# Performance work log

Hardware: AMD Instinct MI355X
Metric: run time of the kernel (lower is better)

## Reference

```python
import jax, jax.numpy as jnp
import numpy as np

B, NQ, NN, EMB, H, D = 64, 256, 512, 128, 8, 16
SQRT_EMB = float(np.sqrt(EMB))
LOGIT_CLIP = 10.0


def setup_inputs() -> dict:
    key = jax.random.key(0)
    ks = jax.random.split(key, 9)
    encoded_last_node = jax.random.normal(ks[0], (B, NQ, EMB), jnp.float32)
    attr = jax.random.uniform(ks[1], (B, NQ, 1), jnp.float32)  # e.g. remaining load in [0,1]
    encoded_nodes = jax.random.normal(ks[2], (B, NN, EMB), jnp.float32)
    ninf_mask = jnp.where(jax.random.uniform(ks[3], (B, NQ, NN)) < 0.15,
                          -jnp.inf, 0.0).astype(jnp.float32)
    def lin(k, fan_in, fan_out):
        lim = 1.0 / np.sqrt(fan_in)
        return jax.random.uniform(k, (fan_in, fan_out), jnp.float32, -lim, lim)
    Wq_last = lin(ks[4], EMB + 1, H * D)
    Wk = lin(ks[5], EMB, H * D)
    Wv = lin(ks[6], EMB, H * D)
    Wcomb = lin(ks[7], H * D, EMB)
    bcomb = jax.random.uniform(ks[8], (EMB,), jnp.float32, -1.0 / np.sqrt(H * D), 1.0 / np.sqrt(H * D))
    return dict(encoded_last_node=encoded_last_node, attr=attr,
                encoded_nodes=encoded_nodes, ninf_mask=ninf_mask,
                Wq_last=Wq_last, Wk=Wk, Wv=Wv, Wcomb=Wcomb, bcomb=bcomb)


def _heads(x):  # [B, T, H*D] -> [B, H, T, D]
    return x.reshape(x.shape[0], x.shape[1], H, D).transpose(0, 2, 1, 3)


def reference(encoded_last_node, attr, encoded_nodes, ninf_mask,
              Wq_last, Wk, Wv, Wcomb, bcomb):
    # fix fully-masked rows: un-mask index 0 (matches torch mask_inf patch)
    all_inf = jnp.isinf(ninf_mask).all(axis=2)  # [B, NQ]
    ninf_mask = ninf_mask.at[:, :, 0].set(jnp.where(all_inf, 0.0, ninf_mask[:, :, 0]))

    # set_kv
    k = _heads(encoded_nodes @ Wk)  # [B,H,NN,D]
    v = _heads(encoded_nodes @ Wv)  # [B,H,NN,D]

    # q from last node + attr
    q = _heads(jnp.concatenate([encoded_last_node, attr], axis=2) @ Wq_last)  # [B,H,NQ,D]

    # masked multi-head attention
    score = jnp.einsum('bhnd,bhmd->bhnm', q, k) / jnp.sqrt(jnp.float32(D))
    score = score + ninf_mask[:, None, :, :]          # rank3 mask broadcast over heads
    weights = jax.nn.softmax(score, axis=-1)          # [B,H,NQ,NN]
    out = jnp.einsum('bhnm,bhmd->bhnd', weights, v)
    out_concat = out.transpose(0, 2, 1, 3).reshape(B, NQ, H * D)
    mh_atten_out = out_concat @ Wcomb + bcomb         # [B,NQ,EMB]

    # single-head compatibility score + tanh clip + mask + softmax
    score2 = jnp.einsum('bne,bme->bnm', mh_atten_out, encoded_nodes) / SQRT_EMB
    logits = LOGIT_CLIP * jnp.tanh(score2) + ninf_mask
    probs = jax.nn.softmax(logits, axis=2)            # [B,NQ,NN]
    return probs
```

## Files before the change

kernel.cpp:

```cpp
#include <hip/hip_runtime.h>
#include <math.h>

#define NB    64
#define NQn   256
#define NNn   512
#define HDn   128
#define LOG2E 1.44269504088896340736f
#define INV_SQRT_EMB 0.08838834764831845f

__device__ __forceinline__ float4 ldg4(const float* p) {
    return *reinterpret_cast<const float4*>(p);
}

__global__ __launch_bounds__(256, 2)
void proj_kernel(const float* __restrict__ X,
                 const float* __restrict__ W0, const float* __restrict__ W1,
                 const float* __restrict__ wrow, const float* __restrict__ attr,
                 const float* __restrict__ bias,
                 float* __restrict__ Y0, float* __restrict__ Y1)
{
    __shared__ float Xs[64 * 128];
    __shared__ float Wt[64 * 128];
    const int tid = threadIdx.x;
    const int rg = tid >> 4;
    const int cg = tid & 15;
    const int rowblk = blockIdx.x * 64;
    const int colbase = blockIdx.y * 64;

    #pragma unroll
    for (int i = 0; i < 8; ++i) {
        int idx = tid + 256 * i;
        int r = idx >> 5;
        int c4 = idx & 31;
        float4 v = ldg4(X + (rowblk + r) * 128 + c4 * 4);
        *reinterpret_cast<float4*>(&Xs[r * 128 + ((c4 ^ (r & 7)) << 2)]) = v;
    }

    for (int pass = 0; pass < 2; ++pass) {
        if (pass && (W1 == nullptr)) break;
        const float* W = pass ? W1 : W0;
        float* Y = pass ? Y1 : Y0;
        __syncthreads();
        #pragma unroll
        for (int i = 0; i < 32; ++i) {
            int idx = tid + 256 * i;
            int k = idx >> 6;
            int c = idx & 63;
            float w = W[k * 128 + colbase + c];
            Wt[c * 128 + ((((k >> 2) ^ (c & 7)) << 2) | (k & 3))] = w;
        }
        __syncthreads();

        float acc[4][4];
        #pragma unroll
        for (int r = 0; r < 4; ++r)
            #pragma unroll
            for (int c = 0; c < 4; ++c) acc[r][c] = 0.f;

        const int rsw = rg & 7;
        const int csw = cg & 7;
        #pragma unroll 8
        for (int k4 = 0; k4 < 32; ++k4) {
            float4 a[4], bv[4];
            #pragma unroll
            for (int r = 0; r < 4; ++r)
                a[r] = *reinterpret_cast<const float4*>(&Xs[(rg + 16 * r) * 128 + ((k4 ^ rsw) << 2)]);
            #pragma unroll
            for (int c = 0; c < 4; ++c)
                bv[c] = *reinterpret_cast<const float4*>(&Wt[(cg + 16 * c) * 128 + ((k4 ^ csw) << 2)]);
            #pragma unroll
            for (int r = 0; r < 4; ++r)
                #pragma unroll
                for (int c = 0; c < 4; ++c)
                    acc[r][c] += a[r].x * bv[c].x + a[r].y * bv[c].y
                               + a[r].z * bv[c].z + a[r].w * bv[c].w;
        }

        if (attr != nullptr) {
            #pragma unroll
            for (int r = 0; r < 4; ++r) {
                float av = attr[rowblk + rg + 16 * r];
                #pragma unroll
                for (int c = 0; c < 4; ++c)
                    acc[r][c] += av * wrow[colbase + cg + 16 * c];
            }
        }
        #pragma unroll
        for (int r = 0; r < 4; ++r) {
            int row = rowblk + rg + 16 * r;
            #pragma unroll
            for (int c = 0; c < 4; ++c) {
                int col = colbase + cg + 16 * c;
                float o = acc[r][c];
                if (bias != nullptr) o += bias[col];
                Y[row * 128 + col] = o;
            }
        }
    }
}

__global__ __launch_bounds__(512, 4)
void attn_kernel(const float* __restrict__ Q, const float* __restrict__ K,
                 const float* __restrict__ V, const float* __restrict__ mask,
                 float* __restrict__ P0, float* __restrict__ P1,
                 float* __restrict__ L0, float* __restrict__ L1)
{
    __shared__ float Ks[32 * 128];
    __shared__ float Vs[32 * 128];
    __shared__ float Ms[32 * 64];
    const int tid  = threadIdx.x;
    const int lane = tid & 63;
    const int h    = tid >> 6;
    const int b    = blockIdx.x;
    const int qt   = blockIdx.y;
    const int ns   = blockIdx.z;
    const int q    = qt * 64 + lane;
    const int nb   = ns * 256;

    float qv[16];
    {
        const float* qp = Q + (b * NQn + q) * 128 + h * 16;
        const float sc = 0.25f * LOG2E;
        float4 t0 = ldg4(qp), t1 = ldg4(qp + 4), t2 = ldg4(qp + 8), t3 = ldg4(qp + 12);
        qv[0]=t0.x*sc;  qv[1]=t0.y*sc;  qv[2]=t0.z*sc;  qv[3]=t0.w*sc;
        qv[4]=t1.x*sc;  qv[5]=t1.y*sc;  qv[6]=t1.z*sc;  qv[7]=t1.w*sc;
        qv[8]=t2.x*sc;  qv[9]=t2.y*sc;  qv[10]=t2.z*sc; qv[11]=t2.w*sc;
        qv[12]=t3.x*sc; qv[13]=t3.y*sc; qv[14]=t3.z*sc; qv[15]=t3.w*sc;
    }

    float out[16];
    #pragma unroll
    for (int d = 0; d < 16; ++d) out[d] = 0.f;
    float lsum = 0.f;

    const int srow = tid >> 3;
    const int sn4  = tid & 7;

    for (int t = 0; t < 8; ++t) {
        const int n0 = nb + t * 32;
        __syncthreads();
        {
            int i0 = tid, i1 = tid + 512;
            const float* kg = K + (b * NNn + n0) * 128;
            const float* vg = V + (b * NNn + n0) * 128;
            float4 k0 = ldg4(kg + i0 * 4), k1 = ldg4(kg + i1 * 4);
            float4 v0 = ldg4(vg + i0 * 4), v1 = ldg4(vg + i1 * 4);
            float4 mk = ldg4(mask + (b * NQn + qt * 64 + srow) * NNn + n0 + sn4 * 4);
            *reinterpret_cast<float4*>(&Ks[i0 * 4]) = k0;
            *reinterpret_cast<float4*>(&Ks[i1 * 4]) = k1;
            *reinterpret_cast<float4*>(&Vs[i0 * 4]) = v0;
            *reinterpret_cast<float4*>(&Vs[i1 * 4]) = v1;
            float mks[4] = {mk.x, mk.y, mk.z, mk.w};
            #pragma unroll
            for (int j = 0; j < 4; ++j) {
                int n = sn4 * 4 + j;
                Ms[n * 64 + (srow ^ n)] = mks[j];
            }
        }
        __syncthreads();

        const float* kbase = &Ks[h * 16];
        const float* vbase = &Vs[h * 16];
        #pragma unroll 2
        for (int g = 0; g < 8; ++g) {
            float p[4];
            #pragma unroll
            for (int j = 0; j < 4; ++j) {
                const int n = g * 4 + j;
                const float* kr = kbase + n * 128;
                float kf[16];
                *reinterpret_cast<float4*>(&kf[0])  = *reinterpret_cast<const float4*>(kr);
                *reinterpret_cast<float4*>(&kf[4])  = *reinterpret_cast<const float4*>(kr + 4);
                *reinterpret_cast<float4*>(&kf[8])  = *reinterpret_cast<const float4*>(kr + 8);
                *reinterpret_cast<float4*>(&kf[12]) = *reinterpret_cast<const float4*>(kr + 12);
                float mv = Ms[n * 64 + (lane ^ n)];
                float sA = qv[0]*kf[0] + qv[1]*kf[1] + qv[2]*kf[2] + qv[3]*kf[3];
                float sB = qv[4]*kf[4] + qv[5]*kf[5] + qv[6]*kf[6] + qv[7]*kf[7];
                float sC = qv[8]*kf[8] + qv[9]*kf[9] + qv[10]*kf[10] + qv[11]*kf[11];
                float sD = qv[12]*kf[12] + qv[13]*kf[13] + qv[14]*kf[14] + qv[15]*kf[15];
                float s = ((sA + sB) + (sC + sD)) + mv;
                p[j] = exp2f(s);
                lsum += p[j];
            }
            #pragma unroll
            for (int j = 0; j < 4; ++j) {
                const int n = g * 4 + j;
                const float* vr = vbase + n * 128;
                float vf[16];
                *reinterpret_cast<float4*>(&vf[0])  = *reinterpret_cast<const float4*>(vr);
                *reinterpret_cast<float4*>(&vf[4])  = *reinterpret_cast<const float4*>(vr + 4);
                *reinterpret_cast<float4*>(&vf[8])  = *reinterpret_cast<const float4*>(vr + 8);
                *reinterpret_cast<float4*>(&vf[12]) = *reinterpret_cast<const float4*>(vr + 12);
                #pragma unroll
                for (int d = 0; d < 16; ++d) out[d] += p[j] * vf[d];
            }
        }
    }

    float* P = ns ? P1 : P0;
    float* L = ns ? L1 : L0;
    float* op = P + (b * NQn + q) * 128 + h * 16;
    *reinterpret_cast<float4*>(op)      = make_float4(out[0],  out[1],  out[2],  out[3]);
    *reinterpret_cast<float4*>(op + 4)  = make_float4(out[4],  out[5],  out[6],  out[7]);
    *reinterpret_cast<float4*>(op + 8)  = make_float4(out[8],  out[9],  out[10], out[11]);
    *reinterpret_cast<float4*>(op + 12) = make_float4(out[12], out[13], out[14], out[15]);
    L[(b * NQn + q) * 8 + h] = lsum;
}

__global__ __launch_bounds__(256, 4)
void attn_merge(const float* __restrict__ P0, const float* __restrict__ P1,
                const float* __restrict__ L0, const float* __restrict__ L1,
                const float* __restrict__ V, float* __restrict__ ATT)
{
    const int idx = blockIdx.x * 256 + threadIdx.x;
    const int row = idx >> 5;
    const int f4i = idx & 31;
    const int hh  = f4i >> 2;
    const int b   = row >> 8;
    const float l = L0[row * 8 + hh] + L1[row * 8 + hh];
    float4 a = ldg4(P0 + row * 128 + f4i * 4);
    float4 c = ldg4(P1 + row * 128 + f4i * 4);
    float4 r;
    if (l == 0.0f) {
        r = ldg4(V + (size_t)b * NNn * 128 + f4i * 4);
    } else {
        float inv = __builtin_amdgcn_rcpf(l);
        r = make_float4((a.x + c.x) * inv, (a.y + c.y) * inv,
                        (a.z + c.z) * inv, (a.w + c.w) * inv);
    }
    *reinterpret_cast<float4*>(ATT + row * 128 + f4i * 4) = r;
}

__global__ __launch_bounds__(512, 2)
void final_kernel(const float* __restrict__ MH, const float* __restrict__ EN,
                  const float* __restrict__ mask, float* __restrict__ OUT)
{
    __shared__ float ENs[128 * 128];
    const int tid = threadIdx.x;
    const int qg = tid >> 4;
    const int mg = tid & 15;
    const int b  = blockIdx.x >> 2;
    const int q0 = (blockIdx.x & 3) * 64;

    const float* mhbase = MH + (b * NQn + q0) * 128;
    float pr[2][32];
    float psum[2] = {0.f, 0.f};
    const int msw = mg & 7;

    #pragma unroll
    for (int t = 0; t < 4; ++t) {
        const int m0 = t * 128;
        __syncthreads();
        #pragma unroll
        for (int i = 0; i < 8; ++i) {
            int idx = tid + 512 * i;
            int r = idx >> 5;
            int c4 = idx & 31;
            float4 v = ldg4(EN + (b * NNn + m0 + r) * 128 + c4 * 4);
            *reinterpret_cast<float4*>(&ENs[r * 128 + ((c4 ^ (r & 7)) << 2)]) = v;
        }
        __syncthreads();

        float acc[2][8];
        #pragma unroll
        for (int qq = 0; qq < 2; ++qq)
            #pragma unroll
            for (int c = 0; c < 8; ++c) acc[qq][c] = 0.f;

        #pragma unroll 4
        for (int k4 = 0; k4 < 32; ++k4) {
            float4 a0 = ldg4(mhbase + (qg * 2 + 0) * 128 + k4 * 4);
            float4 a1 = ldg4(mhbase + (qg * 2 + 1) * 128 + k4 * 4);
            float4 bv[8];
            #pragma unroll
            for (int c = 0; c < 8; ++c)
                bv[c] = *reinterpret_cast<const float4*>(&ENs[(mg + 16 * c) * 128 + ((k4 ^ msw) << 2)]);
            #pragma unroll
            for (int c = 0; c < 8; ++c) {
                acc[0][c] += a0.x*bv[c].x + a0.y*bv[c].y + a0.z*bv[c].z + a0.w*bv[c].w;
                acc[1][c] += a1.x*bv[c].x + a1.y*bv[c].y + a1.z*bv[c].z + a1.w*bv[c].w;
            }
        }

        #pragma unroll
        for (int qq = 0; qq < 2; ++qq) {
            const int q = q0 + qg * 2 + qq;
            const float* mrow = mask + (b * NQn + q) * NNn + m0;
            #pragma unroll
            for (int c = 0; c < 8; ++c) {
                int m = mg + 16 * c;
                float s2 = acc[qq][c] * INV_SQRT_EMB;
                float e  = exp2f(s2 * (2.0f * LOG2E));
                float rc = __builtin_amdgcn_rcpf(e + 1.0f);
                float mv = mrow[m];
                float pv = exp2f((mv - 20.0f * rc) * LOG2E);
                pr[qq][t * 8 + c] = pv;
                psum[qq] += pv;
            }
        }
    }

    #pragma unroll
    for (int qq = 0; qq < 2; ++qq) {
        float s = psum[qq];
        s += __shfl_xor(s, 1);
        s += __shfl_xor(s, 2);
        s += __shfl_xor(s, 4);
        s += __shfl_xor(s, 8);
        psum[qq] = s;
    }

    #pragma unroll
    for (int qq = 0; qq < 2; ++qq) {
        const int q = q0 + qg * 2 + qq;
        float* orow = OUT + (b * NQn + q) * NNn;
        if (psum[qq] == 0.0f) {
            #pragma unroll
            for (int t = 0; t < 4; ++t)
                #pragma unroll
                for (int c = 0; c < 8; ++c) {
                    int m = t * 128 + mg + 16 * c;
                    orow[m] = (m == 0) ? 1.0f : 0.0f;
                }
        } else {
            float inv = __builtin_amdgcn_rcpf(psum[qq]);
            #pragma unroll
            for (int t = 0; t < 4; ++t)
                #pragma unroll
                for (int c = 0; c < 8; ++c)
                    orow[t * 128 + mg + 16 * c] = pr[qq][t * 8 + c] * inv;
        }
    }
}

extern "C" void kernel_launch(void* const* d_in, const int* in_sizes, int n_in,
                              void* d_out, int out_size, void* d_ws, size_t ws_size,
                              hipStream_t stream) {
    const float* enc_last  = (const float*)d_in[0];
    const float* attr      = (const float*)d_in[1];
    const float* enc_nodes = (const float*)d_in[2];
    const float* mask      = (const float*)d_in[3];
    const float* Wq        = (const float*)d_in[4];
    const float* Wk        = (const float*)d_in[5];
    const float* Wv        = (const float*)d_in[6];
    const float* Wcomb     = (const float*)d_in[7];
    const float* bcomb     = (const float*)d_in[8];
    float* out = (float*)d_out;

    float* Kbuf = (float*)d_ws;
    float* Vbuf = Kbuf + (size_t)NB * NNn * 128;
    float* Qbuf = Vbuf + (size_t)NB * NNn * 128;
    float* ATT  = Qbuf + (size_t)NB * NQn * 128;
    float* MH   = ATT  + (size_t)NB * NQn * 128;
    float* P1   = MH   + (size_t)NB * NQn * 128;
    float* L0   = P1   + (size_t)NB * NQn * 128;
    float* L1   = L0   + (size_t)NB * NQn * 8;

    proj_kernel<<<dim3(NB * NNn / 64, 2), 256, 0, stream>>>(
        enc_nodes, Wk, Wv, nullptr, nullptr, nullptr, Kbuf, Vbuf);
    proj_kernel<<<dim3(NB * NQn / 64, 2), 256, 0, stream>>>(
        enc_last, Wq, nullptr, Wq + 128 * 128, attr, nullptr, Qbuf, nullptr);
    attn_kernel<<<dim3(NB, 4, 2), 512, 0, stream>>>(
        Qbuf, Kbuf, Vbuf, mask, ATT, P1, L0, L1);
    attn_merge<<<dim3(NB * NQn * 32 / 256), 256, 0, stream>>>(
        ATT, P1, L0, L1, Vbuf, ATT);
    proj_kernel<<<dim3(NB * NQn / 64, 2), 256, 0, stream>>>(
        ATT, Wcomb, nullptr, nullptr, nullptr, bcomb, MH, nullptr);
    final_kernel<<<dim3(NB * NQn / 64), 512, 0, stream>>>(
        MH, enc_nodes, mask, out);
}
```

Baseline: 245.2 us.

## Register-block four queries per thread and precompute transposed byte mask for attention

The attention kernel now has each thread handle four queries per head, so every K/V row read from shared memory is reused across four queries. Each block covers all 256 queries of a batch and one quarter of the nodes, which raises the split-N partial count from two to four. A new pre-pass transposes the float mask into a byte mask laid out by node, and the kernel applies it by zeroing probabilities instead of adding -inf. This cuts LDS traffic and mask bandwidth, at the cost of an extra kernel, more merge traffic, fewer blocks (256), higher register pressure and lower occupancy.

```diff
diff --git a/kernel.cpp b/kernel.cpp
--- a/kernel.cpp
+++ b/kernel.cpp
@@ -10,6 +10,25 @@
 
 __device__ __forceinline__ float4 ldg4(const float* p) {
     return *reinterpret_cast<const float4*>(p);
+}
+
+__global__ __launch_bounds__(256, 4)
+void mask_transpose(const float* __restrict__ mask, unsigned char* __restrict__ maskT8)
+{
+    const int tid = threadIdx.x;
+    const int w   = tid >> 6;
+    const int n   = blockIdx.z * 64 + (tid & 63);
+    const int b   = blockIdx.x;
+    const int q0  = blockIdx.y * 64 + w * 16;
+    unsigned int u[4] = {0u, 0u, 0u, 0u};
+    #pragma unroll
+    for (int j = 0; j < 16; ++j) {
+        float v = mask[((size_t)(b * NQn + q0 + j)) * NNn + n];
+        unsigned int bit = (v != 0.0f) ? 1u : 0u;
+        u[j >> 2] |= bit << (8 * (j & 3));
+    }
+    *reinterpret_cast<uint4*>(maskT8 + ((size_t)(b * NNn + n)) * NQn + q0) =
+        make_uint4(u[0], u[1], u[2], u[3]);
 }
 
 __global__ __launch_bounds__(256, 2)
@@ -99,117 +118,123 @@
     }
 }
 
-__global__ __launch_bounds__(512, 4)
+__global__ __launch_bounds__(512, 2)
 void attn_kernel(const float* __restrict__ Q, const float* __restrict__ K,
-                 const float* __restrict__ V, const float* __restrict__ mask,
+                 const float* __restrict__ V, const unsigned int* __restrict__ maskTu,
                  float* __restrict__ P0, float* __restrict__ P1,
-                 float* __restrict__ L0, float* __restrict__ L1)
+                 float* __restrict__ P2, float* __restrict__ P3,
+                 float* __restrict__ L0, float* __restrict__ L1,
+                 float* __restrict__ L2, float* __restrict__ L3)
 {
     __shared__ float Ks[32 * 128];
     __shared__ float Vs[32 * 128];
-    __shared__ float Ms[32 * 64];
     const int tid  = threadIdx.x;
     const int lane = tid & 63;
     const int h    = tid >> 6;
     const int b    = blockIdx.x;
-    const int qt   = blockIdx.y;
-    const int ns   = blockIdx.z;
-    const int q    = qt * 64 + lane;
-    const int nb   = ns * 256;
-
-    float qv[16];
+    const int ns   = blockIdx.y;
+    const int nbase = ns * 128;
+
+    float qv[4][16];
     {
-        const float* qp = Q + (b * NQn + q) * 128 + h * 16;
         const float sc = 0.25f * LOG2E;
-        float4 t0 = ldg4(qp), t1 = ldg4(qp + 4), t2 = ldg4(qp + 8), t3 = ldg4(qp + 12);
-        qv[0]=t0.x*sc;  qv[1]=t0.y*sc;  qv[2]=t0.z*sc;  qv[3]=t0.w*sc;
-        qv[4]=t1.x*sc;  qv[5]=t1.y*sc;  qv[6]=t1.z*sc;  qv[7]=t1.w*sc;
-        qv[8]=t2.x*sc;  qv[9]=t2.y*sc;  qv[10]=t2.z*sc; qv[11]=t2.w*sc;
-        qv[12]=t3.x*sc; qv[13]=t3.y*sc; qv[14]=t3.z*sc; qv[15]=t3.w*sc;
-    }
-
-    float out[16];
-    #pragma unroll
-    for (int d = 0; d < 16; ++d) out[d] = 0.f;
-    float lsum = 0.f;
-
-    const int srow = tid >> 3;
-    const int sn4  = tid & 7;
-
-    for (int t = 0; t < 8; ++t) {
-        const int n0 = nb + t * 32;
+        #pragma unroll
+        for (int qq = 0; qq < 4; ++qq) {
+            const float* qp = Q + ((size_t)(b * NQn + 4 * lane + qq)) * 128 + h * 16;
+            #pragma unroll
+            for (int j = 0; j < 4; ++j) {
+                float4 tv = ldg4(qp + 4 * j);
+                qv[qq][4 * j + 0] = tv.x * sc;
+                qv[qq][4 * j + 1] = tv.y * sc;
+                qv[qq][4 * j + 2] = tv.z * sc;
+                qv[qq][4 * j + 3] = tv.w * sc;
+            }
+        }
+    }
+
+    float out[4][16];
+    #pragma unroll
+    for (int qq = 0; qq < 4; ++qq)
+        #pragma unroll
+        for (int d = 0; d < 16; ++d) out[qq][d] = 0.f;
+    float ls[4] = {0.f, 0.f, 0.f, 0.f};
+
+    const unsigned int* mbase = maskTu + (((size_t)(b * NNn + nbase) * NQn) >> 2) + lane;
+
+    for (int t = 0; t < 4; ++t) {
         __syncthreads();
         {
-            int i0 = tid, i1 = tid + 512;
-            const float* kg = K + (b * NNn + n0) * 128;
-            const float* vg = V + (b * NNn + n0) * 128;
-            float4 k0 = ldg4(kg + i0 * 4), k1 = ldg4(kg + i1 * 4);
-            float4 v0 = ldg4(vg + i0 * 4), v1 = ldg4(vg + i1 * 4);
-            float4 mk = ldg4(mask + (b * NQn + qt * 64 + srow) * NNn + n0 + sn4 * 4);
-            *reinterpret_cast<float4*>(&Ks[i0 * 4]) = k0;
-            *reinterpret_cast<float4*>(&Ks[i1 * 4]) = k1;
-            *reinterpret_cast<float4*>(&Vs[i0 * 4]) = v0;
-            *reinterpret_cast<float4*>(&Vs[i1 * 4]) = v1;
-            float mks[4] = {mk.x, mk.y, mk.z, mk.w};
-            #pragma unroll
-            for (int j = 0; j < 4; ++j) {
-                int n = sn4 * 4 + j;
-                Ms[n * 64 + (srow ^ n)] = mks[j];
-            }
+            const float* kg = K + ((size_t)(b * NNn + nbase + t * 32)) * 128;
+            const float* vg = V + ((size_t)(b * NNn + nbase + t * 32)) * 128;
+            float4 k0 = ldg4(kg + tid * 4);
+            float4 k1 = ldg4(kg + (tid + 512) * 4);
+            float4 v0 = ldg4(vg + tid * 4);
+            float4 v1 = ldg4(vg + (tid + 512) * 4);
+            *reinterpret_cast<float4*>(&Ks[tid * 4]) = k0;
+            *reinterpret_cast<float4*>(&Ks[(tid + 512) * 4]) = k1;
+            *reinterpret_cast<float4*>(&Vs[tid * 4]) = v0;
+            *reinterpret_cast<float4*>(&Vs[(tid + 512) * 4]) = v1;
         }
         __syncthreads();
 
         const float* kbase = &Ks[h * 16];
         const float* vbase = &Vs[h * 16];
-        #pragma unroll 2
-        for (int g = 0; g < 8; ++g) {
+        for (int n = 0; n < 32; ++n) {
+            const float* kr = kbase + n * 128;
+            const float* vr = vbase + n * 128;
+            float kf[16], vf[16];
+            *reinterpret_cast<float4*>(&kf[0])  = *reinterpret_cast<const float4*>(kr);
+            *reinterpret_cast<float4*>(&kf[4])  = *reinterpret_cast<const float4*>(kr + 4);
+            *reinterpret_cast<float4*>(&kf[8])  = *reinterpret_cast<const float4*>(kr + 8);
+            *reinterpret_cast<float4*>(&kf[12]) = *reinterpret_cast<const float4*>(kr + 12);
+            *reinterpret_cast<float4*>(&vf[0])  = *reinterpret_cast<const float4*>(vr);
+            *reinterpret_cast<float4*>(&vf[4])  = *reinterpret_cast<const float4*>(vr + 4);
+            *reinterpret_cast<float4*>(&vf[8])  = *reinterpret_cast<const float4*>(vr + 8);
+            *reinterpret_cast<float4*>(&vf[12]) = *reinterpret_cast<const float4*>(vr + 12);
+            unsigned int m4 = mbase[(t * 32 + n) * (NQn / 4)];
+
             float p[4];
             #pragma unroll
-            for (int j = 0; j < 4; ++j) {
-                const int n = g * 4 + j;
-                const float* kr = kbase + n * 128;
-                float kf[16];
-                *reinterpret_cast<float4*>(&kf[0])  = *reinterpret_cast<const float4*>(kr);
-                *reinterpret_cast<float4*>(&kf[4])  = *reinterpret_cast<const float4*>(kr + 4);
-                *reinterpret_cast<float4*>(&kf[8])  = *reinterpret_cast<const float4*>(kr + 8);
-                *reinterpret_cast<float4*>(&kf[12]) = *reinterpret_cast<const float4*>(kr + 12);
-                float mv = Ms[n * 64 + (lane ^ n)];
-                float sA = qv[0]*kf[0] + qv[1]*kf[1] + qv[2]*kf[2] + qv[3]*kf[3];
-                float sB = qv[4]*kf[4] + qv[5]*kf[5] + qv[6]*kf[6] + qv[7]*kf[7];
-                float sC = qv[8]*kf[8] + qv[9]*kf[9] + qv[10]*kf[10] + qv[11]*kf[11];
-                float sD = qv[12]*kf[12] + qv[13]*kf[13] + qv[14]*kf[14] + qv[15]*kf[15];
-                float s = ((sA + sB) + (sC + sD)) + mv;
-                p[j] = exp2f(s);
-                lsum += p[j];
-            }
-            #pragma unroll
-            for (int j = 0; j < 4; ++j) {
-                const int n = g * 4 + j;
-                const float* vr = vbase + n * 128;
-                float vf[16];
-                *reinterpret_cast<float4*>(&vf[0])  = *reinterpret_cast<const float4*>(vr);
-                *reinterpret_cast<float4*>(&vf[4])  = *reinterpret_cast<const float4*>(vr + 4);
-                *reinterpret_cast<float4*>(&vf[8])  = *reinterpret_cast<const float4*>(vr + 8);
-                *reinterpret_cast<float4*>(&vf[12]) = *reinterpret_cast<const float4*>(vr + 12);
-                #pragma unroll
-                for (int d = 0; d < 16; ++d) out[d] += p[j] * vf[d];
-            }
-        }
-    }
-
-    float* P = ns ? P1 : P0;
-    float* L = ns ? L1 : L0;
-    float* op = P + (b * NQn + q) * 128 + h * 16;
-    *reinterpret_cast<float4*>(op)      = make_float4(out[0],  out[1],  out[2],  out[3]);
-    *reinterpret_cast<float4*>(op + 4)  = make_float4(out[4],  out[5],  out[6],  out[7]);
-    *reinterpret_cast<float4*>(op + 8)  = make_float4(out[8],  out[9],  out[10], out[11]);
-    *reinterpret_cast<float4*>(op + 12) = make_float4(out[12], out[13], out[14], out[15]);
-    L[(b * NQn + q) * 8 + h] = lsum;
+            for (int qq = 0; qq < 4; ++qq) {
+                float aP = qv[qq][0]*kf[0] + qv[qq][1]*kf[1] + qv[qq][2]*kf[2] + qv[qq][3]*kf[3];
+                float aQ = qv[qq][4]*kf[4] + qv[qq][5]*kf[5] + qv[qq][6]*kf[6] + qv[qq][7]*kf[7];
+                float aR = qv[qq][8]*kf[8] + qv[qq][9]*kf[9] + qv[qq][10]*kf[10] + qv[qq][11]*kf[11];
+                float aS = qv[qq][12]*kf[12] + qv[qq][13]*kf[13] + qv[qq][14]*kf[14] + qv[qq][15]*kf[15];
+                p[qq] = exp2f((aP + aQ) + (aR + aS));
+            }
+            p[0] = (m4 & 0x000000ffu) ? 0.f : p[0];
+            p[1] = (m4 & 0x0000ff00u) ? 0.f : p[1];
+            p[2] = (m4 & 0x00ff0000u) ? 0.f : p[2];
+            p[3] = (m4 & 0xff000000u) ? 0.f : p[3];
+            ls[0] += p[0]; ls[1] += p[1]; ls[2] += p[2]; ls[3] += p[3];
+            #pragma unroll
+            for (int d = 0; d < 16; ++d) {
+                out[0][d] += p[0] * vf[d];
+                out[1][d] += p[1] * vf[d];
+                out[2][d] += p[2] * vf[d];
+                out[3][d] += p[3] * vf[d];
+            }
+        }
+    }
+
+    float* P = (ns == 0) ? P0 : (ns == 1) ? P1 : (ns == 2) ? P2 : P3;
+    float* L = (ns == 0) ? L0 : (ns == 1) ? L1 : (ns == 2) ? L2 : L3;
+    #pragma unroll
+    for (int qq = 0; qq < 4; ++qq) {
+        float* op = P + ((size_t)(b * NQn + 4 * lane + qq)) * 128 + h * 16;
+        *reinterpret_cast<float4*>(op)      = make_float4(out[qq][0],  out[qq][1],  out[qq][2],  out[qq][3]);
+        *reinterpret_cast<float4*>(op + 4)  = make_float4(out[qq][4],  out[qq][5],  out[qq][6],  out[qq][7]);
+        *reinterpret_cast<float4*>(op + 8)  = make_float4(out[qq][8],  out[qq][9],  out[qq][10], out[qq][11]);
+        *reinterpret_cast<float4*>(op + 12) = make_float4(out[qq][12], out[qq][13], out[qq][14], out[qq][15]);
+        L[(b * NQn + 4 * lane + qq) * 8 + h] = ls[qq];
+    }
 }
 
 __global__ __launch_bounds__(256, 4)
 void attn_merge(const float* __restrict__ P0, const float* __restrict__ P1,
+                const float* __restrict__ P2, const float* __restrict__ P3,
                 const float* __restrict__ L0, const float* __restrict__ L1,
+                const float* __restrict__ L2, const float* __restrict__ L3,
                 const float* __restrict__ V, float* __restrict__ ATT)
 {
     const int idx = blockIdx.x * 256 + threadIdx.x;
@@ -217,18 +242,21 @@
     const int f4i = idx & 31;
     const int hh  = f4i >> 2;
     const int b   = row >> 8;
-    const float l = L0[row * 8 + hh] + L1[row * 8 + hh];
-    float4 a = ldg4(P0 + row * 128 + f4i * 4);
-    float4 c = ldg4(P1 + row * 128 + f4i * 4);
+    const float l = (L0[row * 8 + hh] + L1[row * 8 + hh])
+                  + (L2[row * 8 + hh] + L3[row * 8 + hh]);
+    float4 a = ldg4(P0 + (size_t)row * 128 + f4i * 4);
+    float4 c = ldg4(P1 + (size_t)row * 128 + f4i * 4);
+    float4 d = ldg4(P2 + (size_t)row * 128 + f4i * 4);
+    float4 e = ldg4(P3 + (size_t)row * 128 + f4i * 4);
     float4 r;
     if (l == 0.0f) {
         r = ldg4(V + (size_t)b * NNn * 128 + f4i * 4);
     } else {
         float inv = __builtin_amdgcn_rcpf(l);
-        r = make_float4((a.x + c.x) * inv, (a.y + c.y) * inv,
-                        (a.z + c.z) * inv, (a.w + c.w) * inv);
-    }
-    *reinterpret_cast<float4*>(ATT + row * 128 + f4i * 4) = r;
+        r = make_float4((a.x + c.x + d.x + e.x) * inv, (a.y + c.y + d.y + e.y) * inv,
+                        (a.z + c.z + d.z + e.z) * inv, (a.w + c.w + d.w + e.w) * inv);
+    }
+    *reinterpret_cast<float4*>(ATT + (size_t)row * 128 + f4i * 4) = r;
 }
 
 __global__ __launch_bounds__(512, 2)
@@ -351,19 +379,26 @@
     float* Vbuf = Kbuf + (size_t)NB * NNn * 128;
     float* Qbuf = Vbuf + (size_t)NB * NNn * 128;
     float* ATT  = Qbuf + (size_t)NB * NQn * 128;
-    float* MH   = ATT  + (size_t)NB * NQn * 128;
-    float* P1   = MH   + (size_t)NB * NQn * 128;
-    float* L0   = P1   + (size_t)NB * NQn * 128;
+    float* P1   = ATT  + (size_t)NB * NQn * 128;
+    float* P2   = P1   + (size_t)NB * NQn * 128;
+    float* P3   = P2   + (size_t)NB * NQn * 128;
+    float* L0   = P3   + (size_t)NB * NQn * 128;
     float* L1   = L0   + (size_t)NB * NQn * 8;
-
+    float* L2   = L1   + (size_t)NB * NQn * 8;
+    float* L3   = L2   + (size_t)NB * NQn * 8;
+    unsigned char* maskT8 = (unsigned char*)(L3 + (size_t)NB * NQn * 8);
+    float* MH   = P1;
+
+    mask_transpose<<<dim3(NB, NQn / 64, NNn / 64), 256, 0, stream>>>(mask, maskT8);
     proj_kernel<<<dim3(NB * NNn / 64, 2), 256, 0, stream>>>(
         enc_nodes, Wk, Wv, nullptr, nullptr, nullptr, Kbuf, Vbuf);
     proj_kernel<<<dim3(NB * NQn / 64, 2), 256, 0, stream>>>(
         enc_last, Wq, nullptr, Wq + 128 * 128, attr, nullptr, Qbuf, nullptr);
-    attn_kernel<<<dim3(NB, 4, 2), 512, 0, stream>>>(
-        Qbuf, Kbuf, Vbuf, mask, ATT, P1, L0, L1);
+    attn_kernel<<<dim3(NB, 4), 512, 0, stream>>>(
+        Qbuf, Kbuf, Vbuf, (const unsigned int*)maskT8,
+        ATT, P1, P2, P3, L0, L1, L2, L3);
     attn_merge<<<dim3(NB * NQn * 32 / 256), 256, 0, stream>>>(
-        ATT, P1, L0, L1, Vbuf, ATT);
+        ATT, P1, P2, P3, L0, L1, L2, L3, Vbuf, ATT);
     proj_kernel<<<dim3(NB * NQn / 64, 2), 256, 0, stream>>>(
         ATT, Wcomb, nullptr, nullptr, nullptr, bcomb, MH, nullptr);
     final_kernel<<<dim3(NB * NQn / 64), 512, 0, stream>>>(
```

New measurement: 246.7 us. No clear change (+0.6%).
